# Kernel optimization log

Measured on AMD Instinct MI355X. Metric: run time of the kernel, lower is better.

The kernel has to match this reference:

```python
import math
import jax, jax.numpy as jnp
import numpy as np

HIDDEN = 1024
HEADS = 16
HEAD = HIDDEN // HEADS
BUCKET = 32
MAXPOS = 512
REL = 2 * BUCKET - 1
EPS = 1e-7
L, B = 512, 16
STD = math.sqrt(2.0 / (5.0 * HIDDEN))


def _ln(x, g=None, b=None):
    m = x.mean(-1, keepdims=True)
    v = ((x - m) ** 2).mean(-1, keepdims=True)
    y = (x - m) * jax.lax.rsqrt(v + EPS)
    return y if g is None else y * g + b


def _bucket_indices(n):
    # DeBERTa-style log bucket relative positions, shifted to [0, 2*BUCKET-2]
    r = jnp.arange(n)[:, None] - jnp.arange(n)[None, :]
    mid = BUCKET // 2
    abs_pos = jnp.where((r < mid) & (r > -mid), mid - 1,
                        jnp.clip(jnp.abs(r), None, MAXPOS - 1))
    log_pos = jnp.ceil(jnp.log(abs_pos.astype(jnp.float32) / mid)
                       / math.log((MAXPOS - 1) / mid) * (mid - 1)).astype(jnp.int32) + mid
    bucket_pos = jnp.where(abs_pos <= mid, r, log_pos * jnp.sign(r))
    return (BUCKET - 1 + bucket_pos).astype(jnp.int32)


def setup_inputs() -> dict:
    key = jax.random.key(0)
    ks = jax.random.split(key, 8)
    return {
        'hidden_states': jax.random.normal(ks[0], (L, B, HIDDEN), jnp.float32),
        'attention_mask': jax.random.randint(ks[1], (B, 1, 1, L), 0, 2).astype(bool),
        'relative_embedding': jax.random.normal(ks[2], (REL, HIDDEN), jnp.float32),
        'wqk': jax.random.normal(ks[3], (2 * HIDDEN, HIDDEN), jnp.float32) * STD,
        'bqk': jnp.zeros((2 * HIDDEN,), jnp.float32),
        'wv': jax.random.normal(ks[4], (HIDDEN, HIDDEN), jnp.float32) * STD,
        'bv': jnp.zeros((HIDDEN,), jnp.float32),
        'wo': jax.random.normal(ks[5], (HIDDEN, HIDDEN), jnp.float32) * STD,
        'bo': jnp.zeros((HIDDEN,), jnp.float32),
        'ln_g': jnp.ones((HIDDEN,), jnp.float32),
        'ln_b': jnp.zeros((HIDDEN,), jnp.float32),
    }


def reference(hidden_states, attention_mask, relative_embedding,
              wqk, bqk, wv, bv, wo, bo, ln_g, ln_b):
    Lq, Bq, D = hidden_states.shape
    scale = 1.0 / math.sqrt(3 * HEAD)
    h = _ln(hidden_states)                                 # pre LN, no affine
    q, k = jnp.split(h @ wqk.T + bqk, 2, axis=-1)
    v = h @ wv.T + bv
    qpos, kpos = jnp.split(relative_embedding @ wqk.T + bqk, 2, axis=-1)
    qpos = qpos.reshape(REL, HEADS, HEAD)
    kpos = kpos.reshape(REL, HEADS, HEAD)
    # (L,B,D) -> (B,H,L,hd)
    qh = q.reshape(Lq, Bq, HEADS, HEAD).transpose(1, 2, 0, 3)
    kh = k.reshape(Lq, Bq, HEADS, HEAD).transpose(1, 2, 0, 3)
    vh = v.reshape(Lq, Bq, HEADS, HEAD).transpose(1, 2, 0, 3)
    scores = jnp.einsum('bhqd,bhkd->bhqk', qh, kh) * scale       # c2c
    qp = jnp.einsum('bhqd,khd->bhqk', qh, kpos) * scale          # c2p (k over buckets)
    pk = jnp.einsum('bhkd,qhd->bhqk', kh, qpos) * scale          # p2c (q over buckets)
    idx = jnp.broadcast_to(_bucket_indices(Lq), (Bq, HEADS, Lq, Lq))
    scores = scores + jnp.take_along_axis(qp, idx, axis=-1) \
                    + jnp.take_along_axis(pk, idx, axis=-2)
    # masked softmax: mask==True -> -inf before softmax, 0 after
    probs = jax.nn.softmax(jnp.where(attention_mask, -1e9, scores), axis=-1)
    probs = jnp.where(attention_mask, 0.0, probs)
    ctx = jnp.einsum('bhqk,bhkd->bhqd', probs, vh)
    ctx = ctx.transpose(2, 0, 1, 3).reshape(Lq, Bq, D)           # (L,B,D)
    out = ctx @ wo.T + bo
    return _ln(out, ln_g, ln_b)
```

## Files before the change

### kernel.cpp

```cpp
#include <hip/hip_runtime.h>
#include <hip/hip_bf16.h>

#define HID 1024
#define HEADS 16
#define HEAD 64
#define RELN 63
#define SEQ 512
#define BATCH 16
#define NROWS (SEQ*BATCH)
#define MEXT 8320
#define NQKV 3072
#define LNEPS 1e-7f
#define SCALE2 (0.07216878364870323f * 1.4426950408889634f)

typedef __attribute__((ext_vector_type(4))) float  f32x4;
typedef __attribute__((ext_vector_type(8))) short  s16x8;
typedef __attribute__((ext_vector_type(4))) ushort u16x4;

static __device__ __forceinline__ ushort f2bf(float f) {
  __hip_bfloat16 h = __float2bfloat16(f);
  return *reinterpret_cast<ushort*>(&h);
}
static __device__ __forceinline__ float bf2f(ushort u) {
  union { unsigned u; float f; } v; v.u = ((unsigned)u) << 16;
  return v.f;
}

__global__ void k_prep(const void* mask_raw, const float* bqk, const float* bv,
                       ushort* mask01, int* idx_tab, float* bcat) {
  __shared__ int s_isbool;
  int tid = threadIdx.x;
  if (tid == 0) s_isbool = 0;
  __syncthreads();
  const unsigned* mu = (const unsigned*)mask_raw;
  int bad = 0;
  for (int i = tid; i < 2048; i += 256) if (mu[i] > 1u) bad = 1;
  if (bad) s_isbool = 1;
  __syncthreads();
  int isbool = s_isbool;
  const unsigned char* m8 = (const unsigned char*)mask_raw;
  const int* m32 = (const int*)mask_raw;
  for (int i = tid; i < BATCH*SEQ; i += 256) {
    int m = isbool ? (int)m8[i] : m32[i];
    mask01[i] = m ? 1 : 0;
  }
  for (int i = tid; i < 1023; i += 256) {
    int r = i - 511;
    int a = r < 0 ? -r : r;
    int absp = (a < 16) ? 15 : (a < 511 ? a : 511);
    int idx;
    if (absp <= 16) idx = 31 + r;
    else {
      float v = logf((float)absp / 16.0f) / logf(511.0f / 16.0f) * 15.0f;
      int lp = (int)ceilf(v) + 16;
      idx = 31 + (r > 0 ? lp : -lp);
    }
    idx_tab[i] = idx;
  }
  for (int i = tid; i < 2048; i += 256) bcat[i] = bqk[i];
  for (int i = tid; i < 1024; i += 256) bcat[2048 + i] = bv[i];
}

__global__ __launch_bounds__(256) void k_convert(const float* wqk, const float* wv, const float* wo,
                                                 ushort* wcat, ushort* wo_b) {
  int c = blockIdx.x * 256 + threadIdx.x;
  f32x4 x; ushort* dst;
  if (c < 524288)      { x = *(const f32x4*)(wqk + (size_t)c * 4);            dst = wcat + (size_t)c * 4; }
  else if (c < 786432) { x = *(const f32x4*)(wv  + (size_t)(c - 524288) * 4); dst = wcat + (size_t)c * 4; }
  else                 { x = *(const f32x4*)(wo  + (size_t)(c - 786432) * 4); dst = wo_b + (size_t)(c - 786432) * 4; }
  u16x4 o = { f2bf(x[0]), f2bf(x[1]), f2bf(x[2]), f2bf(x[3]) };
  *(u16x4*)dst = o;
}

__global__ __launch_bounds__(256) void k_ln1(const float* hid, const float* rel, ushort* h_ext) {
  int row = blockIdx.x, tid = threadIdx.x;
  __shared__ float red[8];
  if (row < NROWS) {
    const float* src = hid + (size_t)row * HID;
    f32x4 x = *(const f32x4*)(src + tid * 4);
    float s = x[0] + x[1] + x[2] + x[3];
    #pragma unroll
    for (int m = 1; m < 64; m <<= 1) s += __shfl_xor(s, m);
    if ((tid & 63) == 0) red[tid >> 6] = s;
    __syncthreads();
    float mean = (red[0] + red[1] + red[2] + red[3]) * (1.0f / HID);
    float d0 = x[0] - mean, d1 = x[1] - mean, d2 = x[2] - mean, d3 = x[3] - mean;
    float sq = d0*d0 + d1*d1 + d2*d2 + d3*d3;
    #pragma unroll
    for (int m = 1; m < 64; m <<= 1) sq += __shfl_xor(sq, m);
    __syncthreads();
    if ((tid & 63) == 0) red[4 + (tid >> 6)] = sq;
    __syncthreads();
    float var = (red[4] + red[5] + red[6] + red[7]) * (1.0f / HID);
    float rs = rsqrtf(var + LNEPS);
    u16x4 o = { f2bf(d0*rs), f2bf(d1*rs), f2bf(d2*rs), f2bf(d3*rs) };
    *(u16x4*)(h_ext + (size_t)row * HID + tid * 4) = o;
  } else if (row < NROWS + RELN) {
    const float* src = rel + (size_t)(row - NROWS) * HID;
    f32x4 x = *(const f32x4*)(src + tid * 4);
    u16x4 o = { f2bf(x[0]), f2bf(x[1]), f2bf(x[2]), f2bf(x[3]) };
    *(u16x4*)(h_ext + (size_t)row * HID + tid * 4) = o;
  } else {
    u16x4 z = { 0, 0, 0, 0 };
    *(u16x4*)(h_ext + (size_t)row * HID + tid * 4) = z;
  }
}

__global__ __launch_bounds__(512) void k_gemm256(const ushort* A, const ushort* Bw, const float* bias,
                                                 ushort* Cb, int M, int N, int K) {
  __shared__ char smem[49152];
  char* As = smem;
  char* Bs = smem + 32768;
  int tid = threadIdx.x, lane = tid & 63, w = tid >> 6;
  int nbn = N >> 7;
  int per = gridDim.x >> 3;
  int gl = (blockIdx.x & 7) * per + (blockIdx.x >> 3);
  int bm = gl / nbn, bn = gl % nbn;
  int wr = w >> 1, wc = w & 1;
  int g = lane >> 4, r = lane & 15;
  f32x4 acc[4][4] = {};
  for (int ko = 0; ko < K; ko += 64) {
    __syncthreads();
    #pragma unroll
    for (int c = 0; c < 4; ++c) {
      int chunk = c * 512 + tid;
      int row = chunk >> 3;
      int kbs = ((chunk & 7) << 4) ^ ((row & 7) << 4);
      int ar = bm * 256 + row; ar = ar < M ? ar : M - 1;
      const char* gA = (const char*)(A + (size_t)ar * K + ko) + kbs;
      __builtin_amdgcn_global_load_lds((const __attribute__((address_space(1))) void*)gA,
                                       (__attribute__((address_space(3))) void*)(As + c * 8192 + w * 1024),
                                       16, 0, 0);
    }
    #pragma unroll
    for (int c = 0; c < 2; ++c) {
      int chunk = c * 512 + tid;
      int row = chunk >> 3;
      int kbs = ((chunk & 7) << 4) ^ ((row & 7) << 4);
      const char* gB = (const char*)(Bw + (size_t)(bn * 128 + row) * K + ko) + kbs;
      __builtin_amdgcn_global_load_lds((const __attribute__((address_space(1))) void*)gB,
                                       (__attribute__((address_space(3))) void*)(Bs + c * 8192 + w * 1024),
                                       16, 0, 0);
    }
    __syncthreads();
    #pragma unroll
    for (int kk = 0; kk < 2; ++kk) {
      s16x8 af[4], bf[4];
      #pragma unroll
      for (int mt = 0; mt < 4; ++mt) {
        int row = wr * 64 + mt * 16 + r;
        int kb = (kk * 64 + g * 16) ^ ((row & 7) << 4);
        af[mt] = *(const s16x8*)(As + row * 128 + kb);
      }
      #pragma unroll
      for (int nt = 0; nt < 4; ++nt) {
        int row = wc * 64 + nt * 16 + r;
        int kb = (kk * 64 + g * 16) ^ ((row & 7) << 4);
        bf[nt] = *(const s16x8*)(Bs + row * 128 + kb);
      }
      #pragma unroll
      for (int mt = 0; mt < 4; ++mt)
        #pragma unroll
        for (int nt = 0; nt < 4; ++nt)
          acc[mt][nt] = __builtin_amdgcn_mfma_f32_16x16x32_bf16(af[mt], bf[nt], acc[mt][nt], 0, 0, 0);
    }
  }
  #pragma unroll
  for (int nt = 0; nt < 4; ++nt) {
    int col = bn * 128 + wc * 64 + nt * 16 + r;
    float bvv = bias[col];
    float sc = (col < 1024) ? SCALE2 : 1.0f;
    #pragma unroll
    for (int mt = 0; mt < 4; ++mt) {
      int row0 = bm * 256 + wr * 64 + mt * 16 + g * 4;
      #pragma unroll
      for (int i = 0; i < 4; ++i) {
        int row = row0 + i;
        if (row < M) Cb[(size_t)row * N + col] = f2bf((acc[mt][nt][i] + bvv) * sc);
      }
    }
  }
}

__global__ __launch_bounds__(256) void k_gemm_sk(const ushort* A, const ushort* Bw, const float* bias,
                                                 ushort* C0, ushort* C1) {
  const int N = 1024, K = 1024;
  __shared__ char smem[32768];
  char* As = smem;
  char* Bs = smem + 16384;
  int tid = threadIdx.x, lane = tid & 63, w = tid >> 6;
  int per = gridDim.x >> 3;
  int gl = (blockIdx.x & 7) * per + (blockIdx.x >> 3);
  int bn = gl & 7, ks = (gl >> 3) & 1, bm = gl >> 4;
  int wr = w >> 1, wc = w & 1;
  int g = lane >> 4, r = lane & 15;
  f32x4 acc[4][4] = {};
  for (int ko = ks * 512; ko < ks * 512 + 512; ko += 64) {
    __syncthreads();
    #pragma unroll
    for (int c = 0; c < 4; ++c) {
      int chunk = c * 256 + tid;
      int row = chunk >> 3;
      int kbs = ((chunk & 7) << 4) ^ ((row & 7) << 4);
      const char* gA = (const char*)(A + (size_t)(bm * 128 + row) * K + ko) + kbs;
      const char* gB = (const char*)(Bw + (size_t)(bn * 128 + row) * K + ko) + kbs;
      __builtin_amdgcn_global_load_lds((const __attribute__((address_space(1))) void*)gA,
                                       (__attribute__((address_space(3))) void*)(As + c * 4096 + w * 1024),
                                       16, 0, 0);
      __builtin_amdgcn_global_load_lds((const __attribute__((address_space(1))) void*)gB,
                                       (__attribute__((address_space(3))) void*)(Bs + c * 4096 + w * 1024),
                                       16, 0, 0);
    }
    __syncthreads();
    #pragma unroll
    for (int kk = 0; kk < 2; ++kk) {
      s16x8 af[4], bf[4];
      #pragma unroll
      for (int mt = 0; mt < 4; ++mt) {
        int row = wr * 64 + mt * 16 + r;
        int kb = (kk * 64 + g * 16) ^ ((row & 7) << 4);
        af[mt] = *(const s16x8*)(As + row * 128 + kb);
      }
      #pragma unroll
      for (int nt = 0; nt < 4; ++nt) {
        int row = wc * 64 + nt * 16 + r;
        int kb = (kk * 64 + g * 16) ^ ((row & 7) << 4);
        bf[nt] = *(const s16x8*)(Bs + row * 128 + kb);
      }
      #pragma unroll
      for (int mt = 0; mt < 4; ++mt)
        #pragma unroll
        for (int nt = 0; nt < 4; ++nt)
          acc[mt][nt] = __builtin_amdgcn_mfma_f32_16x16x32_bf16(af[mt], bf[nt], acc[mt][nt], 0, 0, 0);
    }
  }
  ushort* C = ks ? C1 : C0;
  #pragma unroll
  for (int nt = 0; nt < 4; ++nt) {
    int col = bn * 128 + wc * 64 + nt * 16 + r;
    float bvv = ks ? 0.0f : bias[col];
    #pragma unroll
    for (int mt = 0; mt < 4; ++mt) {
      int row0 = bm * 128 + wr * 64 + mt * 16 + g * 4;
      #pragma unroll
      for (int i = 0; i < 4; ++i)
        C[(size_t)(row0 + i) * N + col] = f2bf(acc[mt][nt][i] + bvv);
    }
  }
}

__global__ __launch_bounds__(256) void k_pos(const ushort* qkv, const ushort* mask01,
                                             ushort* qp, ushort* pk) {
  int bh = blockIdx.x;
  int b = bh >> 4, h = bh & 15;
  int tid = threadIdx.x, lane = tid & 63, w = tid >> 6;
  int g = lane >> 4, r = lane & 15;
  __shared__ ushort mb[512];
  for (int i = tid; i < 512; i += 256) mb[i] = mask01[b * SEQ + i];
  __syncthreads();
  s16x8 bkp[4][2], bqp[4][2];
  #pragma unroll
  for (int nt = 0; nt < 4; ++nt)
    #pragma unroll
    for (int kk = 0; kk < 2; ++kk) {
      size_t rowp = (size_t)(NROWS + nt * 16 + r);
      int colq = h * 64 + kk * 32 + g * 8;
      bqp[nt][kk] = *(const s16x8*)(qkv + rowp * NQKV + colq);
      bkp[nt][kk] = *(const s16x8*)(qkv + rowp * NQKV + 1024 + colq);
    }
  for (int cc = 0; cc < 8; ++cc) {
    int rowbase = cc * 64 + w * 16;
    s16x8 aq[2], ak[2];
    #pragma unroll
    for (int kk = 0; kk < 2; ++kk) {
      size_t rowq = (size_t)((rowbase + r) * 16 + b);
      int colq = h * 64 + kk * 32 + g * 8;
      aq[kk] = *(const s16x8*)(qkv + rowq * NQKV + colq);
      ak[kk] = *(const s16x8*)(qkv + rowq * NQKV + 1024 + colq);
    }
    f32x4 accq[4] = {}, acck[4] = {};
    #pragma unroll
    for (int kk = 0; kk < 2; ++kk)
      #pragma unroll
      for (int nt = 0; nt < 4; ++nt) {
        accq[nt] = __builtin_amdgcn_mfma_f32_16x16x32_bf16(aq[kk], bkp[nt][kk], accq[nt], 0, 0, 0);
        acck[nt] = __builtin_amdgcn_mfma_f32_16x16x32_bf16(ak[kk], bqp[nt][kk], acck[nt], 0, 0, 0);
      }
    #pragma unroll
    for (int nt = 0; nt < 4; ++nt)
      #pragma unroll
      for (int i = 0; i < 4; ++i) {
        int q = rowbase + g * 4 + i;
        int t = nt * 16 + r;
        float biasv = mb[q] ? -1e9f : 0.0f;
        qp[(size_t)bh * SEQ * 64 + q * 64 + t] = f2bf(accq[nt][i]);
        pk[(size_t)bh * SEQ * 64 + q * 64 + t] = f2bf(acck[nt][i] + biasv);
      }
  }
}

__global__ __launch_bounds__(256) void k_vt(const ushort* qkv, ushort* vt, ushort* kc) {
  int bid = blockIdx.x;
  int bh = bid >> 3, lt = bid & 7;
  int b = bh >> 4, h = bh & 15;
  __shared__ ushort tile[64][72];
  int tid = threadIdx.x;
  #pragma unroll
  for (int c = 0; c < 2; ++c) {
    int e = (c * 256 + tid) * 8;
    int l = e >> 6, d0 = e & 63;
    size_t row = (size_t)((lt * 64 + l) * 16 + b);
    s16x8 kv = *(const s16x8*)(qkv + row * NQKV + 1024 + h * 64 + d0);
    *(s16x8*)(kc + ((size_t)bh * SEQ + lt * 64 + l) * 64 + d0) = kv;
    *(s16x8*)&tile[l][d0] = *(const s16x8*)(qkv + row * NQKV + 2048 + h * 64 + d0);
  }
  __syncthreads();
  #pragma unroll
  for (int c = 0; c < 2; ++c) {
    int e = (c * 256 + tid) * 8;
    int d = e >> 6, l0 = e & 63;
    ushort tmp[8];
    #pragma unroll
    for (int j = 0; j < 8; ++j) tmp[j] = tile[l0 + j][d];
    *(s16x8*)(vt + (size_t)(bh * 64 + d) * SEQ + lt * 64 + l0) = *(s16x8*)tmp;
  }
}

__global__ __launch_bounds__(512) void k_attn(const ushort* qkv, const ushort* qp_all, const ushort* pk_all,
                                              const ushort* kc, const ushort* vt,
                                              const int* idx_tab, ushort* ctx) {
  int bid = blockIdx.x;
  int slot = bid >> 3;
  int bh = (bid & 7) * 32 + (slot >> 1);
  int qh = slot & 1;
  int b = bh >> 4, h = bh & 15;
  int tid = threadIdx.x, lane = tid & 63, w = tid >> 6;
  int g = lane >> 4, r = lane & 15;

  __shared__ ushort pk_f[512][68];
  __shared__ ushort qp_s[256][68];
  __shared__ ushort p_s[8][16][68];
  __shared__ ushort idx_s[1024];

  const ushort* qpsrc = qp_all + (size_t)bh * SEQ * 64 + (size_t)qh * 256 * 64;
  const ushort* pksrc = pk_all + (size_t)bh * SEQ * 64;
  const char*   kcb   = (const char*)(kc + (size_t)bh * SEQ * 64);

  #pragma unroll
  for (int c = 0; c < 4; ++c) {
    int chunk = c * 512 + tid;
    int row = chunk >> 3, col8 = (chunk & 7) * 8;
    s16x8 v = *(const s16x8*)(qpsrc + (size_t)row * 64 + col8);
    u16x4 lo = { (ushort)v[0], (ushort)v[1], (ushort)v[2], (ushort)v[3] };
    u16x4 hi = { (ushort)v[4], (ushort)v[5], (ushort)v[6], (ushort)v[7] };
    *(u16x4*)&qp_s[row][col8] = lo;
    *(u16x4*)&qp_s[row][col8 + 4] = hi;
  }
  #pragma unroll
  for (int c = 0; c < 8; ++c) {
    int chunk = c * 512 + tid;
    int row = chunk >> 3, col8 = (chunk & 7) * 8;
    s16x8 v = *(const s16x8*)(pksrc + (size_t)row * 64 + col8);
    u16x4 lo = { (ushort)v[0], (ushort)v[1], (ushort)v[2], (ushort)v[3] };
    u16x4 hi = { (ushort)v[4], (ushort)v[5], (ushort)v[6], (ushort)v[7] };
    *(u16x4*)&pk_f[row][col8] = lo;
    *(u16x4*)&pk_f[row][col8 + 4] = hi;
  }
  for (int i = tid; i < 1023; i += 512) idx_s[i] = (ushort)idx_tab[i];
  s16x8 aq[2][2];
  #pragma unroll
  for (int qs = 0; qs < 2; ++qs)
    #pragma unroll
    for (int kk = 0; kk < 2; ++kk) {
      int qglob = qh * 256 + qs * 128 + w * 16 + r;
      aq[qs][kk] = *(const s16x8*)(qkv + ((size_t)qglob * 16 + b) * NQKV + h * 64 + kk * 32 + g * 8);
    }
  __syncthreads();

  float m_i[2] = { -3e38f, -3e38f }, l_i[2] = { 0.0f, 0.0f };
  f32x4 o_acc[2][4] = {};

  for (int kt = 0; kt < 8; ++kt) {
    s16x8 kf[4][2], vf[2][4];
    #pragma unroll
    for (int nt = 0; nt < 4; ++nt)
      #pragma unroll
      for (int kk = 0; kk < 2; ++kk)
        kf[nt][kk] = *(const s16x8*)(kcb + (size_t)(kt * 64 + nt * 16 + r) * 128 + kk * 64 + g * 16);
    #pragma unroll
    for (int kk = 0; kk < 2; ++kk)
      #pragma unroll
      for (int nt = 0; nt < 4; ++nt)
        vf[kk][nt] = *(const s16x8*)(vt + (size_t)(bh * 64 + nt * 16 + r) * SEQ + kt * 64 + kk * 32 + g * 8);

    #pragma unroll
    for (int qs = 0; qs < 2; ++qs) {
      f32x4 s[4];
      __builtin_amdgcn_s_setprio(1);
      #pragma unroll
      for (int nt = 0; nt < 4; ++nt) {
        f32x4 a = {};
        #pragma unroll
        for (int kk = 0; kk < 2; ++kk)
          a = __builtin_amdgcn_mfma_f32_16x16x32_bf16(kf[nt][kk], aq[qs][kk], a, 0, 0, 0);
        s[nt] = a;
      }
      __builtin_amdgcn_s_setprio(0);

      const ushort* qprow = &qp_s[qs * 128 + w * 16 + r][0];
      const int qg511 = qh * 256 + qs * 128 + w * 16 + r + 511;
      float m_loc = -3e38f;
      #pragma unroll
      for (int nt = 0; nt < 4; ++nt) {
        #pragma unroll
        for (int i = 0; i < 4; ++i) {
          int kg = kt * 64 + nt * 16 + g * 4 + i;
          int t = idx_s[qg511 - kg];
          float v = s[nt][i] + bf2f(qprow[t]) + bf2f(pk_f[kg][t]);
          s[nt][i] = v;
          m_loc = fmaxf(m_loc, v);
        }
      }

      float mx = fmaxf(m_loc, __shfl_xor(m_loc, 16));
      mx = fmaxf(mx, __shfl_xor(mx, 32));

      if (__any(mx > m_i[qs] + 8.0f)) {
        float mnew = fmaxf(m_i[qs], mx);
        float rs = exp2f(m_i[qs] - mnew);
        m_i[qs] = mnew;
        l_i[qs] *= rs;
        float rsb[4];
        #pragma unroll
        for (int i = 0; i < 4; ++i) rsb[i] = __shfl(rs, g * 4 + i);
        #pragma unroll
        for (int nt = 0; nt < 4; ++nt)
          #pragma unroll
          for (int i = 0; i < 4; ++i) o_acc[qs][nt][i] *= rsb[i];
      }

      float psum = 0.0f;
      #pragma unroll
      for (int nt = 0; nt < 4; ++nt) {
        u16x4 pk4;
        #pragma unroll
        for (int i = 0; i < 4; ++i) {
          float pe = exp2f(s[nt][i] - m_i[qs]);
          psum += pe;
          pk4[i] = f2bf(pe);
        }
        *(u16x4*)&p_s[w][r][nt * 16 + g * 4] = pk4;
      }
      psum += __shfl_xor(psum, 16);
      psum += __shfl_xor(psum, 32);
      l_i[qs] += psum;

      __builtin_amdgcn_s_setprio(1);
      #pragma unroll
      for (int kk = 0; kk < 2; ++kk) {
        u16x4 lo = *(const u16x4*)&p_s[w][r][kk * 32 + g * 8];
        u16x4 hi = *(const u16x4*)&p_s[w][r][kk * 32 + g * 8 + 4];
        s16x8 pa = { (short)lo[0], (short)lo[1], (short)lo[2], (short)lo[3],
                     (short)hi[0], (short)hi[1], (short)hi[2], (short)hi[3] };
        #pragma unroll
        for (int nt = 0; nt < 4; ++nt)
          o_acc[qs][nt] = __builtin_amdgcn_mfma_f32_16x16x32_bf16(pa, vf[kk][nt], o_acc[qs][nt], 0, 0, 0);
      }
      __builtin_amdgcn_s_setprio(0);
    }
  }

  #pragma unroll
  for (int qs = 0; qs < 2; ++qs) {
    float lb[4];
    #pragma unroll
    for (int i = 0; i < 4; ++i) lb[i] = __shfl(l_i[qs], g * 4 + i);
    #pragma unroll
    for (int i = 0; i < 4; ++i) {
      float inv = lb[i] > 0.0f ? 1.0f / lb[i] : 0.0f;
      int lq = qh * 256 + qs * 128 + w * 16 + g * 4 + i;
      size_t rowc = (size_t)(lq * 16 + b);
      #pragma unroll
      for (int nt = 0; nt < 4; ++nt)
        ctx[rowc * HID + h * 64 + nt * 16 + r] = f2bf(o_acc[qs][nt][i] * inv);
    }
  }
}

__global__ __launch_bounds__(256) void k_ln2(const ushort* t0, const ushort* t1,
                                             const float* gamma, const float* beta, float* out) {
  int row = blockIdx.x, tid = threadIdx.x;
  __shared__ float red[8];
  u16x4 xa = *(const u16x4*)(t0 + (size_t)row * HID + tid * 4);
  u16x4 xb = *(const u16x4*)(t1 + (size_t)row * HID + tid * 4);
  float x[4];
  #pragma unroll
  for (int j = 0; j < 4; ++j) x[j] = bf2f(xa[j]) + bf2f(xb[j]);
  float s = x[0] + x[1] + x[2] + x[3];
  #pragma unroll
  for (int m = 1; m < 64; m <<= 1) s += __shfl_xor(s, m);
  if ((tid & 63) == 0) red[tid >> 6] = s;
  __syncthreads();
  float mean = (red[0] + red[1] + red[2] + red[3]) * (1.0f / HID);
  float d[4]; float sq = 0.0f;
  #pragma unroll
  for (int j = 0; j < 4; ++j) { d[j] = x[j] - mean; sq += d[j] * d[j]; }
  #pragma unroll
  for (int m = 1; m < 64; m <<= 1) sq += __shfl_xor(sq, m);
  __syncthreads();
  if ((tid & 63) == 0) red[4 + (tid >> 6)] = sq;
  __syncthreads();
  float var = (red[4] + red[5] + red[6] + red[7]) * (1.0f / HID);
  float rs = rsqrtf(var + LNEPS);
  f32x4 o;
  #pragma unroll
  for (int j = 0; j < 4; ++j) o[j] = d[j] * rs * gamma[tid * 4 + j] + beta[tid * 4 + j];
  *(f32x4*)(out + (size_t)row * HID + tid * 4) = o;
}

extern "C" void kernel_launch(void* const* d_in, const int* in_sizes, int n_in,
                              void* d_out, int out_size, void* d_ws, size_t ws_size,
                              hipStream_t stream) {
  (void)in_sizes; (void)n_in; (void)out_size; (void)ws_size;
  const float* hid  = (const float*)d_in[0];
  const void*  mask = d_in[1];
  const float* rel  = (const float*)d_in[2];
  const float* wqk  = (const float*)d_in[3];
  const float* bqk  = (const float*)d_in[4];
  const float* wv   = (const float*)d_in[5];
  const float* bv   = (const float*)d_in[6];
  const float* wo   = (const float*)d_in[7];
  const float* bo   = (const float*)d_in[8];
  const float* ln_g = (const float*)d_in[9];
  const float* ln_b = (const float*)d_in[10];

  char* ws = (char*)d_ws;
  ushort* wcat     = (ushort*)(ws);
  ushort* wo_b     = (ushort*)(ws + 6291456);
  float*  bcat     = (float*) (ws + 8388608);
  ushort* mask01   = (ushort*)(ws + 8400896);
  int*    idx_tab  = (int*)   (ws + 8433664);
  ushort* h_ext    = (ushort*)(ws + 8437760);
  ushort* qkv      = (ushort*)(ws + 25477120);
  ushort* qp_b     = (ushort*)(ws + 76595200);
  ushort* pk_b     = (ushort*)(ws + 93372416);
  ushort* vt       = (ushort*)(ws + 110149632);
  char*   tmpr     = (ws + 126926848);
  ushort* ctx = h_ext;
  ushort* kc   = (ushort*)tmpr;
  ushort* tmp0 = (ushort*)tmpr;
  ushort* tmp1 = (ushort*)(tmpr + 16777216);

  k_prep<<<1, 256, 0, stream>>>(mask, bqk, bv, mask01, idx_tab, bcat);
  k_convert<<<4096, 256, 0, stream>>>(wqk, wv, wo, wcat, wo_b);
  k_ln1<<<MEXT, 256, 0, stream>>>(hid, rel, h_ext);
  k_gemm256<<<33 * (NQKV / 128), 512, 0, stream>>>(h_ext, wcat, bcat, qkv, MEXT, NQKV, 1024);
  k_pos<<<256, 256, 0, stream>>>(qkv, mask01, qp_b, pk_b);
  k_vt<<<2048, 256, 0, stream>>>(qkv, vt, kc);
  k_attn<<<512, 512, 0, stream>>>(qkv, qp_b, pk_b, kc, vt, idx_tab, ctx);
  k_gemm_sk<<<1024, 256, 0, stream>>>(ctx, wo_b, bo, tmp0, tmp1);
  k_ln2<<<NROWS, 256, 0, stream>>>(tmp0, tmp1, ln_g, ln_b, (float*)d_out);
}
```

Measured before the change: 250.2 us.

## Split attention blocks to 128 queries each and halve pk shared tile

Each attention block now handles 128 query rows instead of 256, which doubles the grid to 1024 blocks and drops the per-thread two-slice loop, cutting register use. The pk table in shared memory shrinks to 256 rows and is reloaded halfway through the key loop, behind two extra barriers, and the launch bound now requests 4 blocks per CU. Together these lower LDS and register pressure so more waves can be resident. The cost is that K/V tiles and pk data are read from global memory twice as often across blocks, plus the mid-loop reload stall.

```diff
diff --git a/kernel.cpp b/kernel.cpp
--- a/kernel.cpp
+++ b/kernel.cpp
@@ -326,28 +326,28 @@
   }
 }
 
-__global__ __launch_bounds__(512) void k_attn(const ushort* qkv, const ushort* qp_all, const ushort* pk_all,
-                                              const ushort* kc, const ushort* vt,
-                                              const int* idx_tab, ushort* ctx) {
+__global__ __launch_bounds__(512, 4) void k_attn(const ushort* qkv, const ushort* qp_all, const ushort* pk_all,
+                                                 const ushort* kc, const ushort* vt,
+                                                 const int* idx_tab, ushort* ctx) {
   int bid = blockIdx.x;
   int slot = bid >> 3;
-  int bh = (bid & 7) * 32 + (slot >> 1);
-  int qh = slot & 1;
+  int bh = (bid & 7) * 32 + (slot >> 2);
+  int qq = slot & 3;
   int b = bh >> 4, h = bh & 15;
   int tid = threadIdx.x, lane = tid & 63, w = tid >> 6;
   int g = lane >> 4, r = lane & 15;
 
-  __shared__ ushort pk_f[512][68];
-  __shared__ ushort qp_s[256][68];
+  __shared__ ushort pk_s[256][68];
+  __shared__ ushort qp_s[128][68];
   __shared__ ushort p_s[8][16][68];
   __shared__ ushort idx_s[1024];
 
-  const ushort* qpsrc = qp_all + (size_t)bh * SEQ * 64 + (size_t)qh * 256 * 64;
+  const ushort* qpsrc = qp_all + (size_t)bh * SEQ * 64 + (size_t)qq * 128 * 64;
   const ushort* pksrc = pk_all + (size_t)bh * SEQ * 64;
   const char*   kcb   = (const char*)(kc + (size_t)bh * SEQ * 64);
 
   #pragma unroll
-  for (int c = 0; c < 4; ++c) {
+  for (int c = 0; c < 2; ++c) {
     int chunk = c * 512 + tid;
     int row = chunk >> 3, col8 = (chunk & 7) * 8;
     s16x8 v = *(const s16x8*)(qpsrc + (size_t)row * 64 + col8);
@@ -357,30 +357,44 @@
     *(u16x4*)&qp_s[row][col8 + 4] = hi;
   }
   #pragma unroll
-  for (int c = 0; c < 8; ++c) {
+  for (int c = 0; c < 4; ++c) {
     int chunk = c * 512 + tid;
     int row = chunk >> 3, col8 = (chunk & 7) * 8;
     s16x8 v = *(const s16x8*)(pksrc + (size_t)row * 64 + col8);
     u16x4 lo = { (ushort)v[0], (ushort)v[1], (ushort)v[2], (ushort)v[3] };
     u16x4 hi = { (ushort)v[4], (ushort)v[5], (ushort)v[6], (ushort)v[7] };
-    *(u16x4*)&pk_f[row][col8] = lo;
-    *(u16x4*)&pk_f[row][col8 + 4] = hi;
+    *(u16x4*)&pk_s[row][col8] = lo;
+    *(u16x4*)&pk_s[row][col8 + 4] = hi;
   }
   for (int i = tid; i < 1023; i += 512) idx_s[i] = (ushort)idx_tab[i];
-  s16x8 aq[2][2];
-  #pragma unroll
-  for (int qs = 0; qs < 2; ++qs)
-    #pragma unroll
-    for (int kk = 0; kk < 2; ++kk) {
-      int qglob = qh * 256 + qs * 128 + w * 16 + r;
-      aq[qs][kk] = *(const s16x8*)(qkv + ((size_t)qglob * 16 + b) * NQKV + h * 64 + kk * 32 + g * 8);
-    }
-  __syncthreads();
-
-  float m_i[2] = { -3e38f, -3e38f }, l_i[2] = { 0.0f, 0.0f };
-  f32x4 o_acc[2][4] = {};
+  s16x8 aq[2];
+  int qrow = qq * 128 + w * 16 + r;
+  #pragma unroll
+  for (int kk = 0; kk < 2; ++kk)
+    aq[kk] = *(const s16x8*)(qkv + ((size_t)qrow * 16 + b) * NQKV + h * 64 + kk * 32 + g * 8);
+  __syncthreads();
+
+  float m_i = -3e38f, l_i = 0.0f;
+  f32x4 o_acc[4] = {};
+  const ushort* qprow = &qp_s[w * 16 + r][0];
+  const int qg511 = qrow + 511;
 
   for (int kt = 0; kt < 8; ++kt) {
+    if (kt == 4) {
+      __syncthreads();
+      #pragma unroll
+      for (int c = 0; c < 4; ++c) {
+        int chunk = c * 512 + tid;
+        int row = chunk >> 3, col8 = (chunk & 7) * 8;
+        s16x8 v = *(const s16x8*)(pksrc + (size_t)(256 + row) * 64 + col8);
+        u16x4 lo = { (ushort)v[0], (ushort)v[1], (ushort)v[2], (ushort)v[3] };
+        u16x4 hi = { (ushort)v[4], (ushort)v[5], (ushort)v[6], (ushort)v[7] };
+        *(u16x4*)&pk_s[row][col8] = lo;
+        *(u16x4*)&pk_s[row][col8 + 4] = hi;
+      }
+      __syncthreads();
+    }
+
     s16x8 kf[4][2], vf[2][4];
     #pragma unroll
     for (int nt = 0; nt < 4; ++nt)
@@ -393,97 +407,89 @@
       for (int nt = 0; nt < 4; ++nt)
         vf[kk][nt] = *(const s16x8*)(vt + (size_t)(bh * 64 + nt * 16 + r) * SEQ + kt * 64 + kk * 32 + g * 8);
 
-    #pragma unroll
-    for (int qs = 0; qs < 2; ++qs) {
-      f32x4 s[4];
-      __builtin_amdgcn_s_setprio(1);
-      #pragma unroll
-      for (int nt = 0; nt < 4; ++nt) {
-        f32x4 a = {};
+    f32x4 s[4];
+    __builtin_amdgcn_s_setprio(1);
+    #pragma unroll
+    for (int nt = 0; nt < 4; ++nt) {
+      f32x4 a = {};
+      #pragma unroll
+      for (int kk = 0; kk < 2; ++kk)
+        a = __builtin_amdgcn_mfma_f32_16x16x32_bf16(kf[nt][kk], aq[kk], a, 0, 0, 0);
+      s[nt] = a;
+    }
+    __builtin_amdgcn_s_setprio(0);
+
+    float m_loc = -3e38f;
+    #pragma unroll
+    for (int nt = 0; nt < 4; ++nt) {
+      #pragma unroll
+      for (int i = 0; i < 4; ++i) {
+        int kg = kt * 64 + nt * 16 + g * 4 + i;
+        int t = idx_s[qg511 - kg];
+        float v = s[nt][i] + bf2f(qprow[t]) + bf2f(pk_s[kg & 255][t]);
+        s[nt][i] = v;
+        m_loc = fmaxf(m_loc, v);
+      }
+    }
+
+    float mx = fmaxf(m_loc, __shfl_xor(m_loc, 16));
+    mx = fmaxf(mx, __shfl_xor(mx, 32));
+
+    if (__any(mx > m_i + 8.0f)) {
+      float mnew = fmaxf(m_i, mx);
+      float rs = exp2f(m_i - mnew);
+      m_i = mnew;
+      l_i *= rs;
+      float rsb[4];
+      #pragma unroll
+      for (int i = 0; i < 4; ++i) rsb[i] = __shfl(rs, g * 4 + i);
+      #pragma unroll
+      for (int nt = 0; nt < 4; ++nt)
         #pragma unroll
-        for (int kk = 0; kk < 2; ++kk)
-          a = __builtin_amdgcn_mfma_f32_16x16x32_bf16(kf[nt][kk], aq[qs][kk], a, 0, 0, 0);
-        s[nt] = a;
-      }
-      __builtin_amdgcn_s_setprio(0);
-
-      const ushort* qprow = &qp_s[qs * 128 + w * 16 + r][0];
-      const int qg511 = qh * 256 + qs * 128 + w * 16 + r + 511;
-      float m_loc = -3e38f;
-      #pragma unroll
-      for (int nt = 0; nt < 4; ++nt) {
-        #pragma unroll
-        for (int i = 0; i < 4; ++i) {
-          int kg = kt * 64 + nt * 16 + g * 4 + i;
-          int t = idx_s[qg511 - kg];
-          float v = s[nt][i] + bf2f(qprow[t]) + bf2f(pk_f[kg][t]);
-          s[nt][i] = v;
-          m_loc = fmaxf(m_loc, v);
-        }
-      }
-
-      float mx = fmaxf(m_loc, __shfl_xor(m_loc, 16));
-      mx = fmaxf(mx, __shfl_xor(mx, 32));
-
-      if (__any(mx > m_i[qs] + 8.0f)) {
-        float mnew = fmaxf(m_i[qs], mx);
-        float rs = exp2f(m_i[qs] - mnew);
-        m_i[qs] = mnew;
-        l_i[qs] *= rs;
-        float rsb[4];
-        #pragma unroll
-        for (int i = 0; i < 4; ++i) rsb[i] = __shfl(rs, g * 4 + i);
-        #pragma unroll
-        for (int nt = 0; nt < 4; ++nt)
-          #pragma unroll
-          for (int i = 0; i < 4; ++i) o_acc[qs][nt][i] *= rsb[i];
-      }
-
-      float psum = 0.0f;
-      #pragma unroll
-      for (int nt = 0; nt < 4; ++nt) {
-        u16x4 pk4;
-        #pragma unroll
-        for (int i = 0; i < 4; ++i) {
-          float pe = exp2f(s[nt][i] - m_i[qs]);
-          psum += pe;
-          pk4[i] = f2bf(pe);
-        }
-        *(u16x4*)&p_s[w][r][nt * 16 + g * 4] = pk4;
-      }
-      psum += __shfl_xor(psum, 16);
-      psum += __shfl_xor(psum, 32);
-      l_i[qs] += psum;
-
-      __builtin_amdgcn_s_setprio(1);
-      #pragma unroll
-      for (int kk = 0; kk < 2; ++kk) {
-        u16x4 lo = *(const u16x4*)&p_s[w][r][kk * 32 + g * 8];
-        u16x4 hi = *(const u16x4*)&p_s[w][r][kk * 32 + g * 8 + 4];
-        s16x8 pa = { (short)lo[0], (short)lo[1], (short)lo[2], (short)lo[3],
-                     (short)hi[0], (short)hi[1], (short)hi[2], (short)hi[3] };
-        #pragma unroll
-        for (int nt = 0; nt < 4; ++nt)
-          o_acc[qs][nt] = __builtin_amdgcn_mfma_f32_16x16x32_bf16(pa, vf[kk][nt], o_acc[qs][nt], 0, 0, 0);
-      }
-      __builtin_amdgcn_s_setprio(0);
-    }
-  }
-
-  #pragma unroll
-  for (int qs = 0; qs < 2; ++qs) {
-    float lb[4];
-    #pragma unroll
-    for (int i = 0; i < 4; ++i) lb[i] = __shfl(l_i[qs], g * 4 + i);
-    #pragma unroll
-    for (int i = 0; i < 4; ++i) {
-      float inv = lb[i] > 0.0f ? 1.0f / lb[i] : 0.0f;
-      int lq = qh * 256 + qs * 128 + w * 16 + g * 4 + i;
-      size_t rowc = (size_t)(lq * 16 + b);
+        for (int i = 0; i < 4; ++i) o_acc[nt][i] *= rsb[i];
+    }
+
+    float psum = 0.0f;
+    #pragma unroll
+    for (int nt = 0; nt < 4; ++nt) {
+      u16x4 pk4;
+      #pragma unroll
+      for (int i = 0; i < 4; ++i) {
+        float pe = exp2f(s[nt][i] - m_i);
+        psum += pe;
+        pk4[i] = f2bf(pe);
+      }
+      *(u16x4*)&p_s[w][r][nt * 16 + g * 4] = pk4;
+    }
+    psum += __shfl_xor(psum, 16);
+    psum += __shfl_xor(psum, 32);
+    l_i += psum;
+
+    __builtin_amdgcn_s_setprio(1);
+    #pragma unroll
+    for (int kk = 0; kk < 2; ++kk) {
+      u16x4 lo = *(const u16x4*)&p_s[w][r][kk * 32 + g * 8];
+      u16x4 hi = *(const u16x4*)&p_s[w][r][kk * 32 + g * 8 + 4];
+      s16x8 pa = { (short)lo[0], (short)lo[1], (short)lo[2], (short)lo[3],
+                   (short)hi[0], (short)hi[1], (short)hi[2], (short)hi[3] };
       #pragma unroll
       for (int nt = 0; nt < 4; ++nt)
-        ctx[rowc * HID + h * 64 + nt * 16 + r] = f2bf(o_acc[qs][nt][i] * inv);
-    }
+        o_acc[nt] = __builtin_amdgcn_mfma_f32_16x16x32_bf16(pa, vf[kk][nt], o_acc[nt], 0, 0, 0);
+    }
+    __builtin_amdgcn_s_setprio(0);
+  }
+
+  float lb[4];
+  #pragma unroll
+  for (int i = 0; i < 4; ++i) lb[i] = __shfl(l_i, g * 4 + i);
+  #pragma unroll
+  for (int i = 0; i < 4; ++i) {
+    float inv = lb[i] > 0.0f ? 1.0f / lb[i] : 0.0f;
+    int lq = qq * 128 + w * 16 + g * 4 + i;
+    size_t rowc = (size_t)(lq * 16 + b);
+    #pragma unroll
+    for (int nt = 0; nt < 4; ++nt)
+      ctx[rowc * HID + h * 64 + nt * 16 + r] = f2bf(o_acc[nt][i] * inv);
   }
 }
 
@@ -557,7 +563,7 @@
   k_gemm256<<<33 * (NQKV / 128), 512, 0, stream>>>(h_ext, wcat, bcat, qkv, MEXT, NQKV, 1024);
   k_pos<<<256, 256, 0, stream>>>(qkv, mask01, qp_b, pk_b);
   k_vt<<<2048, 256, 0, stream>>>(qkv, vt, kc);
-  k_attn<<<512, 512, 0, stream>>>(qkv, qp_b, pk_b, kc, vt, idx_tab, ctx);
+  k_attn<<<1024, 512, 0, stream>>>(qkv, qp_b, pk_b, kc, vt, idx_tab, ctx);
   k_gemm_sk<<<1024, 256, 0, stream>>>(ctx, wo_b, bo, tmp0, tmp1);
   k_ln2<<<NROWS, 256, 0, stream>>>(tmp0, tmp1, ln_g, ln_b, (float*)d_out);
 }
```

New measurement: 295.7 us. +18.2%, slower.
